# Kernel optimization log

Hardware: AMD Instinct MI355X
Metric: run time of the kernel (lower is better)

The kernel has to match this reference:

```python
import jax, jax.numpy as jnp
import numpy as np

B, N, H, V, STEP = 16, 50, 128, 40000, 2

def setup_inputs() -> dict:
    key = jax.random.key(0)
    ks = jax.random.split(key, 24)
    def nrm(i, shape, s=0.08):
        return jax.random.normal(ks[i], shape, jnp.float32) * s
    items = jax.random.randint(ks[0], (B, N), 0, V)
    A = jax.random.uniform(ks[1], (B, N, 2 * N), jnp.float32)
    lengths = jax.random.randint(ks[2], (B,), 1, N + 1)
    mask = (jnp.arange(N)[None, :] < lengths[:, None]).astype(jnp.int32)
    emb = nrm(3, (V, H), 0.1).at[0].set(0.0)  # padding_idx=0 row zeroed
    return dict(
        items=items, A=A, mask=mask, emb=emb,
        w_ih=nrm(4, (3 * H, 2 * H)), w_hh=nrm(5, (3 * H, H)),
        b_ih=nrm(6, (3 * H,)), b_hh=nrm(7, (3 * H,)),
        b_iah=nrm(8, (H,)), b_oah=nrm(9, (H,)),
        W_ein=nrm(10, (H, H)), b_ein=nrm(11, (H,)),
        W_eout=nrm(12, (H, H)), b_eout=nrm(13, (H,)),
        W_one=nrm(14, (H, H)), b_one=nrm(15, (H,)),
        W_two=nrm(16, (H, H)), b_two=nrm(17, (H,)),
        w_three=nrm(18, (H,)),
        W_tr=nrm(19, (H, 2 * H)), b_tr=nrm(20, (H,)),
        W_t=nrm(21, (H, H)),
    )

def gnn_cell(A, hidden, w_ih, w_hh, b_ih, b_hh, b_iah, b_oah, W_ein, b_ein, W_eout, b_eout):
    # A: [B,N,2N], hidden: [B,N,H]
    ein = hidden @ W_ein.T + b_ein
    eout = hidden @ W_eout.T + b_eout
    input_in = jnp.einsum('bnm,bmh->bnh', A[:, :, :N], ein) + b_iah
    input_out = jnp.einsum('bnm,bmh->bnh', A[:, :, N:], eout) + b_oah
    inputs = jnp.concatenate([input_in, input_out], axis=-1)  # [B,N,2H]
    gi = inputs @ w_ih.T + b_ih
    gh = hidden @ w_hh.T + b_hh
    i_r, i_i, i_n = jnp.split(gi, 3, axis=-1)
    h_r, h_i, h_n = jnp.split(gh, 3, axis=-1)
    resetgate = jax.nn.sigmoid(i_r + h_r)
    inputgate = jax.nn.sigmoid(i_i + h_i)
    newgate = jnp.tanh(i_n + resetgate * h_n)
    return newgate + inputgate * (hidden - newgate)

def reference(items, A, mask, emb, w_ih, w_hh, b_ih, b_hh, b_iah, b_oah,
              W_ein, b_ein, W_eout, b_eout, W_one, b_one, W_two, b_two,
              w_three, W_tr, b_tr, W_t):
    hidden = emb[items]  # [B,N,H]
    for _ in range(STEP):
        hidden = gnn_cell(A, hidden, w_ih, w_hh, b_ih, b_hh, b_iah, b_oah,
                          W_ein, b_ein, W_eout, b_eout)
    # compute_scores
    lengths = jnp.sum(mask, axis=1)  # all >= 1 by construction
    ht = hidden[jnp.arange(B), lengths - 1]  # [B,H] last valid item
    q1 = (ht @ W_one.T + b_one)[:, None, :]
    q2 = hidden @ W_two.T + b_two
    mexp = mask[..., None].astype(jnp.float32)  # [B,N,1]
    alpha_logits = jax.nn.sigmoid(q1 + q2) @ w_three[:, None]  # [B,N,1]
    alpha = jax.nn.softmax(jnp.where(mexp == 0, -jnp.inf, alpha_logits), axis=1)
    a = jnp.sum(alpha * hidden * mexp, axis=1)  # [B,H]
    a = jnp.concatenate([a, ht], axis=1) @ W_tr.T + b_tr  # hybrid (nonhybrid=False)
    b_emb = emb[1:]  # [V-1,H]
    qt = (hidden * mexp) @ W_t.T  # [B,N,H]
    beta_logits = jnp.einsum('vh,bnh->bvn', b_emb, qt)
    beta_logits = jnp.where(mask[:, None, :] == 0, -jnp.inf, beta_logits)
    beta = jax.nn.softmax(beta_logits, axis=-1)  # [B,V-1,N]
    target = jnp.einsum('bvn,bnh->bvh', beta, qt * mexp)  # [B,V-1,H]
    # scores = sum((a[:,None,:] + target) * b_emb, -1), split to avoid extra buffer
    scores = jnp.einsum('bvh,vh->bv', target, b_emb) + a @ b_emb.T
    return scores  # [B, V-1]
```

## Files before the change

### kernel.cpp

```cpp
#include <hip/hip_runtime.h>

#define BB 16
#define NN 50
#define HH 128
#define VV 40000
#define VO 39999

typedef unsigned short u16;
typedef unsigned int u32;
typedef __attribute__((ext_vector_type(8))) short short8;
typedef __attribute__((ext_vector_type(4))) float f32x4;

#define OFF_HID    0
#define OFF_HID2   102400
#define OFF_Q2     102400
#define OFF_Q1     204800
#define OFF_HT     206848
#define OFF_WTWOT  208896
#define OFF_WTT    225280
#define OFF_WONET  241664
#define OFF_WTRT   258048
#define OFF_WEINT  290816
#define OFF_QTBF   307200
#define OFF_WEOUTT 372736
#define OFF_LEN    411648
#define OFF_HA     411664
#define OFF_WHHT   616464
#define OFF_HASUM  665616

__device__ __forceinline__ float sigm(float x){ return 1.0f/(1.0f+__expf(-x)); }
__device__ __forceinline__ float b2f(u16 u){
  union { u32 i; float f; } c; c.i = ((u32)u) << 16; return c.f;
}
__device__ __forceinline__ u16 f2b(float f){
  union { float f; u32 i; } c; c.f = f;
  u32 u = c.i;
  return (u16)((u + 0x7fffu + ((u >> 16) & 1u)) >> 16);
}
__device__ __forceinline__ int frag_idx(int b, int n, int k){
  int tile = n>>4, vlo = n&15, kc = k>>5, quad = (k>>3)&3, j = k&7;
  return (((b*4+tile)*4+kc)<<9) + ((quad<<4)+vlo)*8 + j;
}

__global__ void k_pre(const int* __restrict__ items, const float* __restrict__ emb,
                      const float* __restrict__ W_two, const float* __restrict__ W_t,
                      const float* __restrict__ W_one, const float* __restrict__ W_tr,
                      const float* __restrict__ W_ein, const float* __restrict__ W_eout,
                      const float* __restrict__ w_hh, float* __restrict__ ws){
  int idx = blockIdx.x*256 + threadIdx.x;
  if (idx < 102400){
    int r = idx >> 7, h = idx & 127;
    ws[OFF_HID + idx] = emb[items[r]*128 + h];
  } else if (idx < 118784){
    int i = idx-102400; int k=i>>7, h=i&127;
    ws[OFF_WTWOT + i] = W_two[h*128 + k];
  } else if (idx < 135168){
    int i = idx-118784; int k=i>>7, h=i&127;
    ws[OFF_WTT + i] = W_t[h*128 + k];
  } else if (idx < 151552){
    int i = idx-135168; int k=i>>7, h=i&127;
    ws[OFF_WONET + i] = W_one[h*128 + k];
  } else if (idx < 184320){
    int i = idx-151552; int k=i>>7, h=i&127;
    ws[OFF_WTRT + i] = W_tr[h*256 + k];
  } else if (idx < 200704){
    int i = idx-184320; int k=i>>7, h=i&127;
    ws[OFF_WEINT + i] = W_ein[h*128 + k];
  } else if (idx < 217088){
    int i = idx-200704; int k=i>>7, h=i&127;
    ws[OFF_WEOUTT + i] = W_eout[h*128 + k];
  } else if (idx < 266240){
    int i = idx-217088; int k=i/384, j=i-k*384;
    ws[OFF_WHHT + i] = w_hh[j*128 + k];
  }
}

__global__ void __launch_bounds__(384) k_ha(const float* __restrict__ A,
                       float* __restrict__ ws, int srcOff){
  __shared__ float hall[50][128];
  __shared__ float arow[4][104];
  int t = threadIdx.x;
  int tile = blockIdx.x, b = blockIdx.y;
  int n0 = tile*4;
  const float* hsrc = ws + srcOff + b*6400;
  for (int o=t; o<1600; o+=384) ((float4*)hall)[o] = ((const float4*)hsrc)[o];
  for (int o=t; o<416; o+=384){
    int r=o/104, c=o-r*104;
    arow[r][c] = (c<100 && n0+r<NN) ? A[(size_t)(b*NN+n0+r)*100 + c] : 0.0f;
  }
  __syncthreads();
  for (int o=t; o<1024; o+=384){
    int r = o>>8, kk = o&255;
    int row = n0 + r;
    if (row < NN){
      int k = kk & 127;
      const float* ar = &arow[r][(kk>>7)*50];
      float acc = 0.0f;
      #pragma unroll 5
      for (int m=0;m<50;m++) acc += ar[m]*hall[m][k];
      ws[OFF_HA + (size_t)(b*NN+row)*256 + kk] = acc;
    }
  }
  if (t < 8){
    int r = t>>1, half = t&1;
    if (n0+r < NN){
      const float* ar = &arow[r][half*50];
      float s = 0.0f;
      for (int m=0;m<50;m++) s += ar[m];
      ws[OFF_HASUM + (b*NN+n0+r)*2 + half] = s;
    }
  }
}

__global__ void __launch_bounds__(512) k_gates(const float* __restrict__ w_ih,
                       const float* __restrict__ b_ein, const float* __restrict__ b_eout,
                       const float* __restrict__ b_iah, const float* __restrict__ b_oah,
                       const float* __restrict__ b_ih, const float* __restrict__ b_hh,
                       float* __restrict__ ws, int srcOff, int dstOff){
  __shared__ float h4[4][128];
  __shared__ float ha4[4][256];
  __shared__ float sa4[4][2];
  __shared__ float inp4[4][256];
  __shared__ float gil[4][384];
  __shared__ float ghl[4][384];
  __shared__ float wtile[16][384];
  int t = threadIdx.x;
  int g0 = blockIdx.x*4;
  h4[t>>7][t&127] = ws[srcOff + g0*128 + t];
  ha4[t>>8][t&255] = ws[OFF_HA + g0*256 + t];
  { int o2 = t+512; ha4[o2>>8][o2&255] = ws[OFF_HA + g0*256 + o2]; }
  if (t < 8) sa4[t>>1][t&1] = ws[OFF_HASUM + g0*2 + t];
  __syncthreads();
  {
    int c8 = t & 255, rb = t >> 8;
    int in_half = (c8 < 128) ? 1 : 0;
    int c = c8 & 127;
    const float* wT = ws + (in_half ? OFF_WEINT : OFF_WEOUTT) + c;
    const float* haA = &ha4[rb][in_half ? 0 : 128];
    const float* haB = &ha4[rb+2][in_half ? 0 : 128];
    float a0 = in_half ? (b_iah[c] + sa4[rb  ][0]*b_ein[c]) : (b_oah[c] + sa4[rb  ][1]*b_eout[c]);
    float a1 = in_half ? (b_iah[c] + sa4[rb+2][0]*b_ein[c]) : (b_oah[c] + sa4[rb+2][1]*b_eout[c]);
    for (int k=0;k<128;k+=4){
      float w0=wT[(k+0)*128], w1=wT[(k+1)*128], w2=wT[(k+2)*128], w3=wT[(k+3)*128];
      float4 hA = *(const float4*)(haA + k);
      float4 hB = *(const float4*)(haB + k);
      a0 += hA.x*w0 + hA.y*w1 + hA.z*w2 + hA.w*w3;
      a1 += hB.x*w0 + hB.y*w1 + hB.z*w2 + hB.w*w3;
    }
    inp4[rb][c8] = a0;
    inp4[rb+2][c8] = a1;
  }
  __syncthreads();
  int j = t;
  float gacc0=0,gacc1=0,gacc2=0,gacc3=0;
  if (j < 384){ float bi = b_ih[j]; gacc0=gacc1=gacc2=gacc3=bi; }
  for (int k0=0;k0<256;k0+=16){
    #pragma unroll
    for (int q=0;q<3;q++){
      int u = t + q*512;
      int row = u>>2, seg = u&3;
      float4 v = *(const float4*)(w_ih + row*256 + k0 + seg*4);
      int kb = seg*4;
      wtile[kb+0][row]=v.x; wtile[kb+1][row]=v.y; wtile[kb+2][row]=v.z; wtile[kb+3][row]=v.w;
    }
    __syncthreads();
    if (j < 384){
      #pragma unroll
      for (int kk=0;kk<16;kk++){
        float w = wtile[kk][j];
        gacc0 += w*inp4[0][k0+kk];
        gacc1 += w*inp4[1][k0+kk];
        gacc2 += w*inp4[2][k0+kk];
        gacc3 += w*inp4[3][k0+kk];
      }
    }
    __syncthreads();
  }
  if (j < 384){ gil[0][j]=gacc0; gil[1][j]=gacc1; gil[2][j]=gacc2; gil[3][j]=gacc3; }
  if (j < 384){
    float bh = b_hh[j];
    float q0=bh,q1=bh,q2=bh,q3=bh;
    const float* wT = ws + OFF_WHHT + j;
    for (int k=0;k<128;k+=4){
      float w0=wT[(k+0)*384], w1=wT[(k+1)*384], w2=wT[(k+2)*384], w3=wT[(k+3)*384];
      float4 v0 = *(const float4*)(&h4[0][k]);
      float4 v1 = *(const float4*)(&h4[1][k]);
      float4 v2 = *(const float4*)(&h4[2][k]);
      float4 v3 = *(const float4*)(&h4[3][k]);
      q0 += v0.x*w0 + v0.y*w1 + v0.z*w2 + v0.w*w3;
      q1 += v1.x*w0 + v1.y*w1 + v1.z*w2 + v1.w*w3;
      q2 += v2.x*w0 + v2.y*w1 + v2.z*w2 + v2.w*w3;
      q3 += v3.x*w0 + v3.y*w1 + v3.z*w2 + v3.w*w3;
    }
    ghl[0][j]=q0; ghl[1][j]=q1; ghl[2][j]=q2; ghl[3][j]=q3;
  }
  __syncthreads();
  {
    int r = t>>7, h = t&127;
    float ir_=gil[r][h], ii=gil[r][128+h], inw=gil[r][256+h];
    float hr_=ghl[r][h], hi2=ghl[r][128+h], hn=ghl[r][256+h];
    float rg=sigm(ir_+hr_), ig=sigm(ii+hi2), ng=tanhf(inw+rg*hn);
    float hv=h4[r][h];
    ws[dstOff + (g0+r)*128 + h] = ng + ig*(hv-ng);
  }
}

__global__ void __launch_bounds__(256) k_post(const int* __restrict__ mask,
                      const float* __restrict__ b_two, const float* __restrict__ b_one,
                      float* __restrict__ ws){
  int bx = blockIdx.x, t = threadIdx.x;
  u16* qtbf = (u16*)(ws + OFF_QTBF);
  if (bx < 200){
    bool isq2 = bx < 100;
    int r0 = (isq2 ? bx : bx-100) * 8;
    __shared__ float hl[1024];
    for (int i=0;i<4;i++) hl[t+i*256] = ws[OFF_HID + r0*128 + t + i*256];
    __syncthreads();
    int h = t & 127, g = t >> 7;
    const float* wT = ws + (isq2 ? OFF_WTWOT : OFF_WTT);
    float binit = isq2 ? b_two[h] : 0.0f;
    float acc[4];
    #pragma unroll
    for (int r=0;r<4;r++) acc[r] = binit;
    for (int k4=0;k4<32;k4++){
      int k = k4*4;
      float w0 = wT[(k+0)*128+h], w1 = wT[(k+1)*128+h];
      float w2 = wT[(k+2)*128+h], w3 = wT[(k+3)*128+h];
      #pragma unroll
      for (int r=0;r<4;r++){
        float4 hv = *(const float4*)(hl + (g*4+r)*128 + k);
        acc[r] += hv.x*w0 + hv.y*w1 + hv.z*w2 + hv.w*w3;
      }
    }
    #pragma unroll
    for (int r=0;r<4;r++){
      int row = r0 + g*4 + r;
      if (isq2) ws[OFF_Q2 + row*128 + h] = acc[r];
      else {
        float val = mask[row] ? acc[r] : 0.0f;
        int b = row/NN, n = row - b*NN;
        qtbf[frag_idx(b, n, h)] = f2b(val);
      }
    }
  } else if (bx < 248){
    int i = (bx-200)*256 + t;
    #pragma unroll
    for (int kk=0;kk<2;kk++){
      int e = i*2 + kk;
      int b = e/1536, rem = e - b*1536;
      int kc = rem/384, rem2 = rem - kc*384;
      int quad = rem2/96, vv = rem2 - quad*96;
      int vlo = 4 + vv/8, j = vv & 7;
      qtbf[(((b*4+3)*4+kc)<<9) + ((quad<<4)+vlo)*8 + j] = 0;
    }
  } else {
    __shared__ float htl[128];
    int b = bx - 248;
    if (t < 128){
      int len = 0;
      for (int n=0;n<NN;n++) len += mask[b*NN+n];
      if (len<1) len=1; if (len>NN) len=NN;
      float ht = ws[OFF_HID + (b*NN + len-1)*128 + t];
      ws[OFF_HT + b*128 + t] = ht;
      htl[t] = ht;
      if (t==0) ((int*)(ws+OFF_LEN))[b] = len;
    }
    __syncthreads();
    if (t < 128){
      const float* w1T = ws + OFF_WONET;
      float q1 = b_one[t];
      for (int k=0;k<128;k+=4){
        float4 h4v = *(const float4*)(htl + k);
        q1 += h4v.x*w1T[(k+0)*128+t] + h4v.y*w1T[(k+1)*128+t]
            + h4v.z*w1T[(k+2)*128+t] + h4v.w*w1T[(k+3)*128+t];
      }
      ws[OFF_Q1 + b*128 + t] = q1;
    }
  }
}

__global__ void __launch_bounds__(256) k_attn2(const float* __restrict__ w_three,
                        const float* __restrict__ b_tr, float* __restrict__ ws){
  __shared__ float q2l[NN*129];
  __shared__ float q1l[128], w3l[128], htl[128], al[128], pt2[128], alg[64];
  int t = threadIdx.x;
  int b = blockIdx.x;
  for (int o=t;o<6400;o+=256){ int n=o>>7, h=o&127; q2l[n*129+h] = ws[OFF_Q2 + b*6400 + o]; }
  if (t < 128){
    q1l[t] = ws[OFF_Q1 + b*128 + t];
    w3l[t] = w_three[t];
    htl[t] = ws[OFF_HT + b*128 + t];
  }
  int len = ((const int*)(ws+OFF_LEN))[b];
  __syncthreads();
  if (t < 200){
    int n = t>>2, part = t&3;
    if (n < len){
      const float* qr  = q2l + n*129 + part*32;
      const float* q1p = q1l + part*32;
      const float* w3p = w3l + part*32;
      float s = 0.0f;
      for (int h=0;h<32;h++) s += w3p[h]*sigm(q1p[h]+qr[h]);
      s += __shfl_xor(s,1); s += __shfl_xor(s,2);
      if (part==0) alg[n] = s;
    }
  }
  __syncthreads();
  if (t < 64){
    float v = (t<len) ? alg[t] : -1e30f;
    float m = v;
    m = fmaxf(m, __shfl_xor(m,1));  m = fmaxf(m, __shfl_xor(m,2));
    m = fmaxf(m, __shfl_xor(m,4));  m = fmaxf(m, __shfl_xor(m,8));
    m = fmaxf(m, __shfl_xor(m,16)); m = fmaxf(m, __shfl_xor(m,32));
    float e = (t<len) ? __expf(v - m) : 0.0f;
    float ss = e;
    ss += __shfl_xor(ss,1);  ss += __shfl_xor(ss,2);
    ss += __shfl_xor(ss,4);  ss += __shfl_xor(ss,8);
    ss += __shfl_xor(ss,16); ss += __shfl_xor(ss,32);
    float inv = 1.0f/ss;
    if (t<len) alg[t] = e*inv;
  }
  __syncthreads();
  if (t < 128){
    const float* hid = ws + OFF_HID + b*6400;
    float a = 0.0f;
    for (int n=0;n<len;n++) a += alg[n]*hid[n*128+t];
    al[t] = a;
  }
  __syncthreads();
  float p1 = 0.0f;
  if (t < 256){
    int g2 = t>>7, h = t&127;
    const float* wtr = ws + OFF_WTRT + g2*128*128;
    const float* src = g2 ? htl : al;
    float p = 0.0f;
    for (int k=0;k<128;k++) p += src[k]*wtr[k*128+h];
    if (g2) pt2[h] = p; else p1 = p;
  }
  __syncthreads();
  if (t < 128){
    float af = b_tr[t] + p1 + pt2[t];
    u16 hi = f2b(af);
    u16 lo = f2b(af - b2f(hi));
    u16* qtbf = (u16*)(ws + OFF_QTBF);
    qtbf[frag_idx(b, 50, t)] = hi;
    qtbf[frag_idx(b, 51, t)] = lo;
  }
}

__global__ void __launch_bounds__(256) k_scores(const float* __restrict__ emb,
                                                const float* __restrict__ ws,
                                                float* __restrict__ out){
  __shared__ u16 qlds[8192];
  int tid = threadIdx.x;
  int lane = tid & 63, wave = tid >> 6;
  int quad = lane >> 4, vlo = lane & 15;
  int v = blockIdx.y*64 + wave*16 + vlo;
  int vc = (v < VO) ? v : (VO-1);
  const float* erow = emb + (size_t)(vc+1)*128;
  short8 bfr[4];
  #pragma unroll
  for (int kc=0;kc<4;kc++){
    const float4* p = (const float4*)(erow + kc*32 + quad*8);
    float4 x = p[0], y = p[1];
    union { short8 s; u32 w[4]; } u;
    u.w[0] = (u32)f2b(x.x) | ((u32)f2b(x.y)<<16);
    u.w[1] = (u32)f2b(x.z) | ((u32)f2b(x.w)<<16);
    u.w[2] = (u32)f2b(y.x) | ((u32)f2b(y.y)<<16);
    u.w[3] = (u32)f2b(y.z) | ((u32)f2b(y.w)<<16);
    bfr[kc] = u.s;
  }
  const u16* qtf = (const u16*)(ws + OFF_QTBF);
  const int* slen = (const int*)(ws + OFF_LEN);
  int b0 = blockIdx.x*4;
  for (int bi=0;bi<4;bi++){
    int b = b0 + bi;
    __syncthreads();
    {
      const uint4* src = (const uint4*)qtf + (size_t)b*1024;
      uint4* dst = (uint4*)qlds;
      #pragma unroll
      for (int r=0;r<4;r++) dst[tid + r*256] = src[tid + r*256];
    }
    __syncthreads();
    int len = slen[b];
    f32x4 acc0={0.f,0.f,0.f,0.f}, acc1=acc0, acc2=acc0, acc3=acc0;
    #pragma unroll
    for (int kc=0;kc<4;kc++){
      const u16* base = qlds + kc*512 + lane*8;
      short8 a0 = *(const short8*)(base + 0*2048);
      short8 a1 = *(const short8*)(base + 1*2048);
      short8 a2 = *(const short8*)(base + 2*2048);
      short8 a3 = *(const short8*)(base + 3*2048);
      acc0 = __builtin_amdgcn_mfma_f32_16x16x32_bf16(a0, bfr[kc], acc0, 0,0,0);
      acc1 = __builtin_amdgcn_mfma_f32_16x16x32_bf16(a1, bfr[kc], acc1, 0,0,0);
      acc2 = __builtin_amdgcn_mfma_f32_16x16x32_bf16(a2, bfr[kc], acc2, 0,0,0);
      acc3 = __builtin_amdgcn_mfma_f32_16x16x32_bf16(a3, bfr[kc], acc3, 0,0,0);
    }
    int nb = quad*4;
    float ss=0.f, nm=0.f;
    #pragma unroll
    for (int r=0;r<4;r++){
      { int n=nb+r;    if(n<len){ float e=__expf(acc0[r]); ss+=e; nm+=e*acc0[r]; } }
      { int n=nb+r+16; if(n<len){ float e=__expf(acc1[r]); ss+=e; nm+=e*acc1[r]; } }
      { int n=nb+r+32; if(n<len){ float e=__expf(acc2[r]); ss+=e; nm+=e*acc2[r]; } }
      { int n=nb+r+48; if(n<len){ float e=__expf(acc3[r]); ss+=e; nm+=e*acc3[r]; } }
    }
    ss += __shfl_xor(ss,16); ss += __shfl_xor(ss,32);
    nm += __shfl_xor(nm,16); nm += __shfl_xor(nm,32);
    if (quad==0 && v < VO){
      float pa = acc3[2] + acc3[3];
      out[(size_t)b*VO + v] = nm/ss + pa;
    }
  }
}

extern "C" void kernel_launch(void* const* d_in, const int* in_sizes, int n_in,
                              void* d_out, int out_size, void* d_ws, size_t ws_size,
                              hipStream_t stream){
  const int*   items  = (const int*)d_in[0];
  const float* A      = (const float*)d_in[1];
  const int*   mask   = (const int*)d_in[2];
  const float* emb    = (const float*)d_in[3];
  const float* w_ih   = (const float*)d_in[4];
  const float* w_hh   = (const float*)d_in[5];
  const float* b_ih   = (const float*)d_in[6];
  const float* b_hh   = (const float*)d_in[7];
  const float* b_iah  = (const float*)d_in[8];
  const float* b_oah  = (const float*)d_in[9];
  const float* W_ein  = (const float*)d_in[10];
  const float* b_ein  = (const float*)d_in[11];
  const float* W_eout = (const float*)d_in[12];
  const float* b_eout = (const float*)d_in[13];
  const float* W_one  = (const float*)d_in[14];
  const float* b_one  = (const float*)d_in[15];
  const float* W_two  = (const float*)d_in[16];
  const float* b_two  = (const float*)d_in[17];
  const float* w_three= (const float*)d_in[18];
  const float* W_tr   = (const float*)d_in[19];
  const float* b_tr   = (const float*)d_in[20];
  const float* W_t    = (const float*)d_in[21];
  float* ws  = (float*)d_ws;
  float* out = (float*)d_out;

  k_pre<<<1040,256,0,stream>>>(items,emb,W_two,W_t,W_one,W_tr,W_ein,W_eout,w_hh,ws);
  k_ha   <<<dim3(13,16),384,0,stream>>>(A,ws,OFF_HID);
  k_gates<<<200,512,0,stream>>>(w_ih,b_ein,b_eout,b_iah,b_oah,b_ih,b_hh,ws,OFF_HID,OFF_HID2);
  k_ha   <<<dim3(13,16),384,0,stream>>>(A,ws,OFF_HID2);
  k_gates<<<200,512,0,stream>>>(w_ih,b_ein,b_eout,b_iah,b_oah,b_ih,b_hh,ws,OFF_HID2,OFF_HID);
  k_post <<<264,256,0,stream>>>(mask,b_two,b_one,ws);
  k_attn2<<<16,256,0,stream>>>(w_three,b_tr,ws);
  k_scores<<<dim3(4,625),256,0,stream>>>(emb,ws,out);
}
```

Baseline: 218.9 us.

## Fuse adjacency aggregation kernel into GRU gate kernel per GNN step

Merges k_ha and k_gates into one kernel, k_step2, launched on a (13,16) grid. Each block loads its batch's hidden state and A rows into shared memory, computes the A@hidden aggregation and row sums in shared memory, then runs the gate math. This drops two launches and the global round trip through the HA and HASUM buffers. In exchange, each block reloads the full 50x128 hidden tile, the last tile per batch carries padded rows, and the wtile row is padded to 385 to reduce bank conflicts.

New measurement: 210.6 us, median of 2. 1.04x faster.

```diff
diff --git a/kernel.cpp b/kernel.cpp
--- a/kernel.cpp
+++ b/kernel.cpp
@@ -24,9 +24,7 @@
 #define OFF_QTBF   307200
 #define OFF_WEOUTT 372736
 #define OFF_LEN    411648
-#define OFF_HA     411664
 #define OFF_WHHT   616464
-#define OFF_HASUM  665616
 
 __device__ __forceinline__ float sigm(float x){ return 1.0f/(1.0f+__expf(-x)); }
 __device__ __forceinline__ float b2f(u16 u){
@@ -75,61 +73,46 @@
   }
 }
 
-__global__ void __launch_bounds__(384) k_ha(const float* __restrict__ A,
-                       float* __restrict__ ws, int srcOff){
-  __shared__ float hall[50][128];
-  __shared__ float arow[4][104];
-  int t = threadIdx.x;
-  int tile = blockIdx.x, b = blockIdx.y;
-  int n0 = tile*4;
-  const float* hsrc = ws + srcOff + b*6400;
-  for (int o=t; o<1600; o+=384) ((float4*)hall)[o] = ((const float4*)hsrc)[o];
-  for (int o=t; o<416; o+=384){
-    int r=o/104, c=o-r*104;
-    arow[r][c] = (c<100 && n0+r<NN) ? A[(size_t)(b*NN+n0+r)*100 + c] : 0.0f;
-  }
-  __syncthreads();
-  for (int o=t; o<1024; o+=384){
-    int r = o>>8, kk = o&255;
-    int row = n0 + r;
-    if (row < NN){
-      int k = kk & 127;
-      const float* ar = &arow[r][(kk>>7)*50];
-      float acc = 0.0f;
-      #pragma unroll 5
-      for (int m=0;m<50;m++) acc += ar[m]*hall[m][k];
-      ws[OFF_HA + (size_t)(b*NN+row)*256 + kk] = acc;
-    }
-  }
-  if (t < 8){
-    int r = t>>1, half = t&1;
-    if (n0+r < NN){
-      const float* ar = &arow[r][half*50];
-      float s = 0.0f;
-      for (int m=0;m<50;m++) s += ar[m];
-      ws[OFF_HASUM + (b*NN+n0+r)*2 + half] = s;
-    }
-  }
-}
-
-__global__ void __launch_bounds__(512) k_gates(const float* __restrict__ w_ih,
+__global__ void __launch_bounds__(512) k_step2(const float* __restrict__ A,
+                       const float* __restrict__ w_ih,
                        const float* __restrict__ b_ein, const float* __restrict__ b_eout,
                        const float* __restrict__ b_iah, const float* __restrict__ b_oah,
                        const float* __restrict__ b_ih, const float* __restrict__ b_hh,
                        float* __restrict__ ws, int srcOff, int dstOff){
-  __shared__ float h4[4][128];
+  __shared__ float hall[50][128];
+  __shared__ float arow[4][104];
   __shared__ float ha4[4][256];
   __shared__ float sa4[4][2];
   __shared__ float inp4[4][256];
   __shared__ float gil[4][384];
   __shared__ float ghl[4][384];
-  __shared__ float wtile[16][384];
+  __shared__ float wtile[16][385];
   int t = threadIdx.x;
-  int g0 = blockIdx.x*4;
-  h4[t>>7][t&127] = ws[srcOff + g0*128 + t];
-  ha4[t>>8][t&255] = ws[OFF_HA + g0*256 + t];
-  { int o2 = t+512; ha4[o2>>8][o2&255] = ws[OFF_HA + g0*256 + o2]; }
-  if (t < 8) sa4[t>>1][t&1] = ws[OFF_HASUM + g0*2 + t];
+  int tile = blockIdx.x, b = blockIdx.y;
+  int n0 = tile*4;
+  const float* hsrc = ws + srcOff + b*6400;
+  for (int o=t; o<1600; o+=512) ((float4*)hall)[o] = ((const float4*)hsrc)[o];
+  if (t < 416){
+    int r=t/104, c=t-r*104;
+    arow[r][c] = (c<100 && n0+r<NN) ? A[(size_t)(b*NN+n0+r)*100 + c] : 0.0f;
+  }
+  __syncthreads();
+  for (int o=t; o<1024; o+=512){
+    int r = o>>8, kk = o&255;
+    int k = kk & 127;
+    const float* ar = &arow[r][(kk>>7)*50];
+    float acc = 0.0f;
+    #pragma unroll 5
+    for (int m=0;m<50;m++) acc += ar[m]*hall[m][k];
+    ha4[r][kk] = acc;
+  }
+  if (t < 8){
+    int r = t>>1, half = t&1;
+    const float* ar = &arow[r][half*50];
+    float s = 0.0f;
+    for (int m=0;m<50;m++) s += ar[m];
+    sa4[r][half] = s;
+  }
   __syncthreads();
   {
     int c8 = t & 255, rb = t >> 8;
@@ -181,12 +164,15 @@
     float bh = b_hh[j];
     float q0=bh,q1=bh,q2=bh,q3=bh;
     const float* wT = ws + OFF_WHHT + j;
+    int r1 = (n0+1<NN)? n0+1 : n0;
+    int r2 = (n0+2<NN)? n0+2 : n0;
+    int r3 = (n0+3<NN)? n0+3 : n0;
     for (int k=0;k<128;k+=4){
       float w0=wT[(k+0)*384], w1=wT[(k+1)*384], w2=wT[(k+2)*384], w3=wT[(k+3)*384];
-      float4 v0 = *(const float4*)(&h4[0][k]);
-      float4 v1 = *(const float4*)(&h4[1][k]);
-      float4 v2 = *(const float4*)(&h4[2][k]);
-      float4 v3 = *(const float4*)(&h4[3][k]);
+      float4 v0 = *(const float4*)(&hall[n0][k]);
+      float4 v1 = *(const float4*)(&hall[r1][k]);
+      float4 v2 = *(const float4*)(&hall[r2][k]);
+      float4 v3 = *(const float4*)(&hall[r3][k]);
       q0 += v0.x*w0 + v0.y*w1 + v0.z*w2 + v0.w*w3;
       q1 += v1.x*w0 + v1.y*w1 + v1.z*w2 + v1.w*w3;
       q2 += v2.x*w0 + v2.y*w1 + v2.z*w2 + v2.w*w3;
@@ -196,12 +182,14 @@
   }
   __syncthreads();
   {
-    int r = t>>7, h = t&127;
-    float ir_=gil[r][h], ii=gil[r][128+h], inw=gil[r][256+h];
-    float hr_=ghl[r][h], hi2=ghl[r][128+h], hn=ghl[r][256+h];
-    float rg=sigm(ir_+hr_), ig=sigm(ii+hi2), ng=tanhf(inw+rg*hn);
-    float hv=h4[r][h];
-    ws[dstOff + (g0+r)*128 + h] = ng + ig*(hv-ng);
+    int r = t>>7, h = t&127, row = n0+r;
+    if (row < NN){
+      float ir_=gil[r][h], ii=gil[r][128+h], inw=gil[r][256+h];
+      float hr_=ghl[r][h], hi2=ghl[r][128+h], hn=ghl[r][256+h];
+      float rg=sigm(ir_+hr_), ig=sigm(ii+hi2), ng=tanhf(inw+rg*hn);
+      float hv=hall[row][h];
+      ws[dstOff + (b*NN+row)*128 + h] = ng + ig*(hv-ng);
+    }
   }
 }
 
@@ -444,10 +432,8 @@
   float* out = (float*)d_out;
 
   k_pre<<<1040,256,0,stream>>>(items,emb,W_two,W_t,W_one,W_tr,W_ein,W_eout,w_hh,ws);
-  k_ha   <<<dim3(13,16),384,0,stream>>>(A,ws,OFF_HID);
-  k_gates<<<200,512,0,stream>>>(w_ih,b_ein,b_eout,b_iah,b_oah,b_ih,b_hh,ws,OFF_HID,OFF_HID2);
-  k_ha   <<<dim3(13,16),384,0,stream>>>(A,ws,OFF_HID2);
-  k_gates<<<200,512,0,stream>>>(w_ih,b_ein,b_eout,b_iah,b_oah,b_ih,b_hh,ws,OFF_HID2,OFF_HID);
+  k_step2<<<dim3(13,16),512,0,stream>>>(A,w_ih,b_ein,b_eout,b_iah,b_oah,b_ih,b_hh,ws,OFF_HID,OFF_HID2);
+  k_step2<<<dim3(13,16),512,0,stream>>>(A,w_ih,b_ein,b_eout,b_iah,b_oah,b_ih,b_hh,ws,OFF_HID2,OFF_HID);
   k_post <<<264,256,0,stream>>>(mask,b_two,b_one,ws);
   k_attn2<<<16,256,0,stream>>>(w_three,b_tr,ws);
   k_scores<<<dim3(4,625),256,0,stream>>>(emb,ws,out);
```
